# Kernel optimization log

Hardware: AMD Instinct MI355X
Metric: run time of the kernel (lower is better)

## Reference

```python
import jax, jax.numpy as jnp
import numpy as np

IN_FEATURES = 8192
OUT_FEATURES = 8192
WEIGHT_PER_OUT = 32
BATCH = 1024


def setup_inputs() -> dict:
    key = jax.random.key(0)
    k1, k2, k3 = jax.random.split(key, 3)
    x = jax.random.normal(k1, (BATCH, IN_FEATURES), dtype=jnp.float32)
    connections = jax.random.randint(k2, (OUT_FEATURES, WEIGHT_PER_OUT), 0, IN_FEATURES, dtype=jnp.int32)
    bound = 1.0 / np.sqrt(WEIGHT_PER_OUT)
    weights = jax.random.uniform(k3, (OUT_FEATURES, WEIGHT_PER_OUT), dtype=jnp.float32, minval=-bound, maxval=bound)
    return {"x": x, "connections": connections, "weights": weights}


def reference(x, connections, weights):
    # x: [B, In]; connections, weights: [O, K]
    # out[b, o] = sum_k x[b, connections[o, k]] * weights[o, k]
    gathered = jnp.take(x, connections, axis=1)  # [B, O, K]
    return jnp.einsum('bok,ok->bo', gathered, weights)
```

## Files before the change

### kernel.cpp

```cpp
#include <hip/hip_runtime.h>
#include <hip/hip_fp16.h>


typedef _Float16 half2_t __attribute__((ext_vector_type(2)));

constexpr int IN_F    = 8192;
constexpr int OUT_F   = 8192;
constexpr int KPER    = 32;
constexpr int BATCH   = 1024;
constexpr int ROWS    = 4;
constexpr int THREADS = 1024;
constexpr int OHALF   = OUT_F / 2;
constexpr size_t PK_BYTES = (size_t)OUT_F * (KPER / 4) * 16;

__global__ __launch_bounds__(256)
void psl_repack(const int* __restrict__ conn, const float* __restrict__ w,
                uint4* __restrict__ pk) {
    const int t = blockIdx.x * 256 + threadIdx.x;
    const int j = t >> 13;
    const int o = t & (OUT_F - 1);
    const int base = o * KPER + j * 4;
    const int4   ci = *reinterpret_cast<const int4*>(conn + base);
    const float4 wj = *reinterpret_cast<const float4*>(w + base);
    uint4 v;
    v.x = ((unsigned)ci.x << 3) | ((unsigned)ci.y << 19);
    v.z = ((unsigned)ci.z << 3) | ((unsigned)ci.w << 19);
    __half2 w01 = __floats2half2_rn(wj.x, wj.y);
    __half2 w23 = __floats2half2_rn(wj.z, wj.w);
    v.y = *reinterpret_cast<unsigned*>(&w01);
    v.w = *reinterpret_cast<unsigned*>(&w23);
    pk[(size_t)j * OUT_F + o] = v;
}

__device__ __forceinline__ float dot2acc(unsigned hi, unsigned lo,
                                         unsigned sel, unsigned wbits,
                                         float acc) {
    unsigned p = __builtin_amdgcn_perm(hi, lo, sel);
    return __builtin_amdgcn_fdot2(__builtin_bit_cast(half2_t, p),
                                  __builtin_bit_cast(half2_t, wbits),
                                  acc, false);
}

__global__ __launch_bounds__(THREADS, 8)
void psl_main(const float* __restrict__ x, const uint4* __restrict__ pk,
              float* __restrict__ out) {
    __shared__ uint2 lds_x[IN_F];

    const int tid = threadIdx.x;
    const int bt  = blockIdx.x >> 1;
    const int oh  = blockIdx.x & 1;
    const long b0 = (long)bt * ROWS;

    const float* xr0 = x + (b0 + 0) * IN_F;
    const float* xr1 = x + (b0 + 1) * IN_F;
    const float* xr2 = x + (b0 + 2) * IN_F;
    const float* xr3 = x + (b0 + 3) * IN_F;

    for (int c = tid; c < IN_F; c += THREADS) {
        __half2 h01 = __floats2half2_rn(xr0[c], xr1[c]);
        __half2 h23 = __floats2half2_rn(xr2[c], xr3[c]);
        uint2 pkx;
        pkx.x = *reinterpret_cast<unsigned*>(&h01);
        pkx.y = *reinterpret_cast<unsigned*>(&h23);
        lds_x[c] = pkx;
    }
    __syncthreads();

    float* or0 = out + (b0 + 0) * OUT_F;
    float* or1 = out + (b0 + 1) * OUT_F;
    float* or2 = out + (b0 + 2) * OUT_F;
    float* or3 = out + (b0 + 3) * OUT_F;

    const int obase = oh * OHALF;
    const char* ldsb = reinterpret_cast<const char*>(lds_x);

    for (int jj = 0; jj < OHALF / THREADS; ++jj) {
        const int o = obase + jj * THREADS + tid;
        const uint4* pkrow = pk + o;

        float a0 = 0.f, a1 = 0.f, a2 = 0.f, a3 = 0.f;

#pragma unroll 2
        for (int j = 0; j < KPER / 4; ++j) {
            const uint4 v = pkrow[(size_t)j * OUT_F];
            const unsigned off0 = v.x & 0xFFFFu, off1 = v.x >> 16;
            const unsigned off2 = v.z & 0xFFFFu, off3 = v.z >> 16;
            const uint2 g0 = *reinterpret_cast<const uint2*>(ldsb + off0);
            const uint2 g1 = *reinterpret_cast<const uint2*>(ldsb + off1);
            const uint2 g2 = *reinterpret_cast<const uint2*>(ldsb + off2);
            const uint2 g3 = *reinterpret_cast<const uint2*>(ldsb + off3);
            a0 = dot2acc(g1.x, g0.x, 0x05040100u, v.y, a0);
            a1 = dot2acc(g1.x, g0.x, 0x07060302u, v.y, a1);
            a2 = dot2acc(g1.y, g0.y, 0x05040100u, v.y, a2);
            a3 = dot2acc(g1.y, g0.y, 0x07060302u, v.y, a3);
            a0 = dot2acc(g3.x, g2.x, 0x05040100u, v.w, a0);
            a1 = dot2acc(g3.x, g2.x, 0x07060302u, v.w, a1);
            a2 = dot2acc(g3.y, g2.y, 0x05040100u, v.w, a2);
            a3 = dot2acc(g3.y, g2.y, 0x07060302u, v.w, a3);
        }

        or0[o] = a0;
        or1[o] = a1;
        or2[o] = a2;
        or3[o] = a3;
    }
}

__global__ __launch_bounds__(512, 4)
void psl_fallback(const float* __restrict__ x, const int* __restrict__ conn,
                  const float* __restrict__ w, float* __restrict__ out) {
    __shared__ uint2 lds_x[IN_F];
    const int tid = threadIdx.x;
    const int bt  = blockIdx.x >> 1;
    const int oh  = blockIdx.x & 1;
    const long b0 = (long)bt * ROWS;
    const float* xr0 = x + (b0 + 0) * IN_F;
    const float* xr1 = x + (b0 + 1) * IN_F;
    const float* xr2 = x + (b0 + 2) * IN_F;
    const float* xr3 = x + (b0 + 3) * IN_F;
    for (int c = tid; c < IN_F; c += 512) {
        __half2 h01 = __floats2half2_rn(xr0[c], xr1[c]);
        __half2 h23 = __floats2half2_rn(xr2[c], xr3[c]);
        uint2 pkx;
        pkx.x = *reinterpret_cast<unsigned*>(&h01);
        pkx.y = *reinterpret_cast<unsigned*>(&h23);
        lds_x[c] = pkx;
    }
    __syncthreads();
    float* or0 = out + (b0 + 0) * OUT_F;
    float* or1 = out + (b0 + 1) * OUT_F;
    float* or2 = out + (b0 + 2) * OUT_F;
    float* or3 = out + (b0 + 3) * OUT_F;
    const int obase = oh * OHALF;
    for (int j = 0; j < OHALF / 512; ++j) {
        const int o = obase + j * 512 + tid;
        const int4*   c4 = reinterpret_cast<const int4*>(conn + (size_t)o * KPER);
        const float4* w4 = reinterpret_cast<const float4*>(w + (size_t)o * KPER);
        float a0 = 0.f, a1 = 0.f, a2 = 0.f, a3 = 0.f;
#define GACC(IDX, WT)                                              \
        {                                                          \
            uint2 v = lds_x[(IDX)];                                \
            __half2 h01 = *reinterpret_cast<__half2*>(&v.x);       \
            __half2 h23 = *reinterpret_cast<__half2*>(&v.y);       \
            float2 f01 = __half22float2(h01);                      \
            float2 f23 = __half22float2(h23);                      \
            a0 = fmaf(f01.x, (WT), a0);                            \
            a1 = fmaf(f01.y, (WT), a1);                            \
            a2 = fmaf(f23.x, (WT), a2);                            \
            a3 = fmaf(f23.y, (WT), a3);                            \
        }
#pragma unroll
        for (int jj = 0; jj < KPER / 4; ++jj) {
            const int4   ci = c4[jj];
            const float4 wj = w4[jj];
            GACC(ci.x, wj.x);
            GACC(ci.y, wj.y);
            GACC(ci.z, wj.z);
            GACC(ci.w, wj.w);
        }
#undef GACC
        or0[o] = a0;
        or1[o] = a1;
        or2[o] = a2;
        or3[o] = a3;
    }
}

extern "C" void kernel_launch(void* const* d_in, const int* in_sizes, int n_in,
                              void* d_out, int out_size, void* d_ws, size_t ws_size,
                              hipStream_t stream) {
    const float* x    = (const float*)d_in[0];
    const int*   conn = (const int*)d_in[1];
    const float* w    = (const float*)d_in[2];
    float*       out  = (float*)d_out;

    if (ws_size >= PK_BYTES) {
        uint4* pk = (uint4*)d_ws;
        psl_repack<<<dim3(OUT_F * (KPER / 4) / 256), 256, 0, stream>>>(conn, w, pk);
        psl_main<<<dim3((BATCH / ROWS) * 2), THREADS, 0, stream>>>(x, pk, out);
    } else {
        psl_fallback<<<dim3((BATCH / ROWS) * 2), 512, 0, stream>>>(x, conn, w, out);
    }
}
```

Baseline: 104.2 us.

## Process eight batch rows per block with packed fp16 FMA accumulation

Each block now stages eight batch rows of x into LDS as uint4 per input column, so one gathered LDS read serves eight outputs and the packed connection/weight stream is reused across twice as many rows. The fp32 dot2 accumulation with byte permutes is replaced by packed half2 FMAs that accumulate in fp16, split across two accumulator sets and summed in fp32 at the end. This halves the number of blocks and the re-reads of the packed index stream. In exchange it doubles LDS use to 128KB per block, which lowers occupancy, and fp16 accumulation reduces accuracy.

```diff
diff --git a/kernel.cpp b/kernel.cpp
--- a/kernel.cpp
+++ b/kernel.cpp
@@ -1,14 +1,12 @@
 #include <hip/hip_runtime.h>
 #include <hip/hip_fp16.h>
 
-
-typedef _Float16 half2_t __attribute__((ext_vector_type(2)));
 
 constexpr int IN_F    = 8192;
 constexpr int OUT_F   = 8192;
 constexpr int KPER    = 32;
 constexpr int BATCH   = 1024;
-constexpr int ROWS    = 4;
+constexpr int ROWS    = 8;
 constexpr int THREADS = 1024;
 constexpr int OHALF   = OUT_F / 2;
 constexpr size_t PK_BYTES = (size_t)OUT_F * (KPER / 4) * 16;
@@ -23,86 +21,101 @@
     const int4   ci = *reinterpret_cast<const int4*>(conn + base);
     const float4 wj = *reinterpret_cast<const float4*>(w + base);
     uint4 v;
-    v.x = ((unsigned)ci.x << 3) | ((unsigned)ci.y << 19);
-    v.z = ((unsigned)ci.z << 3) | ((unsigned)ci.w << 19);
+    v.x = (unsigned)ci.x | ((unsigned)ci.y << 16);
+    v.y = (unsigned)ci.z | ((unsigned)ci.w << 16);
     __half2 w01 = __floats2half2_rn(wj.x, wj.y);
     __half2 w23 = __floats2half2_rn(wj.z, wj.w);
-    v.y = *reinterpret_cast<unsigned*>(&w01);
+    v.z = *reinterpret_cast<unsigned*>(&w01);
     v.w = *reinterpret_cast<unsigned*>(&w23);
     pk[(size_t)j * OUT_F + o] = v;
 }
 
-__device__ __forceinline__ float dot2acc(unsigned hi, unsigned lo,
-                                         unsigned sel, unsigned wbits,
-                                         float acc) {
-    unsigned p = __builtin_amdgcn_perm(hi, lo, sel);
-    return __builtin_amdgcn_fdot2(__builtin_bit_cast(half2_t, p),
-                                  __builtin_bit_cast(half2_t, wbits),
-                                  acc, false);
+__device__ __forceinline__ __half2 u2h2(unsigned u) {
+    return __builtin_bit_cast(__half2, u);
+}
+__device__ __forceinline__ unsigned packh2(float a, float b) {
+    __half2 h = __floats2half2_rn(a, b);
+    return *reinterpret_cast<unsigned*>(&h);
 }
 
-__global__ __launch_bounds__(THREADS, 8)
+__global__ __launch_bounds__(THREADS, 4)
 void psl_main(const float* __restrict__ x, const uint4* __restrict__ pk,
               float* __restrict__ out) {
-    __shared__ uint2 lds_x[IN_F];
+    __shared__ uint4 lds_x[IN_F];
 
     const int tid = threadIdx.x;
     const int bt  = blockIdx.x >> 1;
     const int oh  = blockIdx.x & 1;
     const long b0 = (long)bt * ROWS;
 
-    const float* xr0 = x + (b0 + 0) * IN_F;
-    const float* xr1 = x + (b0 + 1) * IN_F;
-    const float* xr2 = x + (b0 + 2) * IN_F;
-    const float* xr3 = x + (b0 + 3) * IN_F;
+    const float* xr = x + b0 * IN_F;
 
     for (int c = tid; c < IN_F; c += THREADS) {
-        __half2 h01 = __floats2half2_rn(xr0[c], xr1[c]);
-        __half2 h23 = __floats2half2_rn(xr2[c], xr3[c]);
-        uint2 pkx;
-        pkx.x = *reinterpret_cast<unsigned*>(&h01);
-        pkx.y = *reinterpret_cast<unsigned*>(&h23);
+        uint4 pkx;
+        pkx.x = packh2(xr[0 * IN_F + c], xr[1 * IN_F + c]);
+        pkx.y = packh2(xr[2 * IN_F + c], xr[3 * IN_F + c]);
+        pkx.z = packh2(xr[4 * IN_F + c], xr[5 * IN_F + c]);
+        pkx.w = packh2(xr[6 * IN_F + c], xr[7 * IN_F + c]);
         lds_x[c] = pkx;
     }
     __syncthreads();
 
-    float* or0 = out + (b0 + 0) * OUT_F;
-    float* or1 = out + (b0 + 1) * OUT_F;
-    float* or2 = out + (b0 + 2) * OUT_F;
-    float* or3 = out + (b0 + 3) * OUT_F;
-
+    float* outb = out + b0 * OUT_F;
     const int obase = oh * OHALF;
-    const char* ldsb = reinterpret_cast<const char*>(lds_x);
 
     for (int jj = 0; jj < OHALF / THREADS; ++jj) {
         const int o = obase + jj * THREADS + tid;
         const uint4* pkrow = pk + o;
 
-        float a0 = 0.f, a1 = 0.f, a2 = 0.f, a3 = 0.f;
+        __half2 z = __float2half2_rn(0.f);
+        __half2 a01 = z, a23 = z, a45 = z, a67 = z;
+        __half2 b01 = z, b23 = z, b45 = z, b67 = z;
 
-#pragma unroll 2
+#pragma unroll
         for (int j = 0; j < KPER / 4; ++j) {
             const uint4 v = pkrow[(size_t)j * OUT_F];
-            const unsigned off0 = v.x & 0xFFFFu, off1 = v.x >> 16;
-            const unsigned off2 = v.z & 0xFFFFu, off3 = v.z >> 16;
-            const uint2 g0 = *reinterpret_cast<const uint2*>(ldsb + off0);
-            const uint2 g1 = *reinterpret_cast<const uint2*>(ldsb + off1);
-            const uint2 g2 = *reinterpret_cast<const uint2*>(ldsb + off2);
-            const uint2 g3 = *reinterpret_cast<const uint2*>(ldsb + off3);
-            a0 = dot2acc(g1.x, g0.x, 0x05040100u, v.y, a0);
-            a1 = dot2acc(g1.x, g0.x, 0x07060302u, v.y, a1);
-            a2 = dot2acc(g1.y, g0.y, 0x05040100u, v.y, a2);
-            a3 = dot2acc(g1.y, g0.y, 0x07060302u, v.y, a3);
-            a0 = dot2acc(g3.x, g2.x, 0x05040100u, v.w, a0);
-            a1 = dot2acc(g3.x, g2.x, 0x07060302u, v.w, a1);
-            a2 = dot2acc(g3.y, g2.y, 0x05040100u, v.w, a2);
-            a3 = dot2acc(g3.y, g2.y, 0x07060302u, v.w, a3);
+            const unsigned i0 = v.x & 0xFFFFu, i1 = v.x >> 16;
+            const unsigned i2 = v.y & 0xFFFFu, i3 = v.y >> 16;
+            const uint4 g0 = lds_x[i0];
+            const uint4 g1 = lds_x[i1];
+            const uint4 g2 = lds_x[i2];
+            const uint4 g3 = lds_x[i3];
+            const __half2 w01 = u2h2(v.z), w23 = u2h2(v.w);
+            const __half2 wd0 = __half2half2(__low2half(w01));
+            const __half2 wd1 = __half2half2(__high2half(w01));
+            const __half2 wd2 = __half2half2(__low2half(w23));
+            const __half2 wd3 = __half2half2(__high2half(w23));
+
+            a01 = __hfma2(u2h2(g0.x), wd0, a01);
+            a23 = __hfma2(u2h2(g0.y), wd0, a23);
+            a45 = __hfma2(u2h2(g0.z), wd0, a45);
+            a67 = __hfma2(u2h2(g0.w), wd0, a67);
+            b01 = __hfma2(u2h2(g1.x), wd1, b01);
+            b23 = __hfma2(u2h2(g1.y), wd1, b23);
+            b45 = __hfma2(u2h2(g1.z), wd1, b45);
+            b67 = __hfma2(u2h2(g1.w), wd1, b67);
+            a01 = __hfma2(u2h2(g2.x), wd2, a01);
+            a23 = __hfma2(u2h2(g2.y), wd2, a23);
+            a45 = __hfma2(u2h2(g2.z), wd2, a45);
+            a67 = __hfma2(u2h2(g2.w), wd2, a67);
+            b01 = __hfma2(u2h2(g3.x), wd3, b01);
+            b23 = __hfma2(u2h2(g3.y), wd3, b23);
+            b45 = __hfma2(u2h2(g3.z), wd3, b45);
+            b67 = __hfma2(u2h2(g3.w), wd3, b67);
         }
 
-        or0[o] = a0;
-        or1[o] = a1;
-        or2[o] = a2;
-        or3[o] = a3;
+        const float2 r01 = __half22float2(a01), s01 = __half22float2(b01);
+        const float2 r23 = __half22float2(a23), s23 = __half22float2(b23);
+        const float2 r45 = __half22float2(a45), s45 = __half22float2(b45);
+        const float2 r67 = __half22float2(a67), s67 = __half22float2(b67);
+        outb[0 * OUT_F + o] = r01.x + s01.x;
+        outb[1 * OUT_F + o] = r01.y + s01.y;
+        outb[2 * OUT_F + o] = r23.x + s23.x;
+        outb[3 * OUT_F + o] = r23.y + s23.y;
+        outb[4 * OUT_F + o] = r45.x + s45.x;
+        outb[5 * OUT_F + o] = r45.y + s45.y;
+        outb[6 * OUT_F + o] = r67.x + s67.x;
+        outb[7 * OUT_F + o] = r67.y + s67.y;
     }
 }
 
@@ -113,17 +126,15 @@
     const int tid = threadIdx.x;
     const int bt  = blockIdx.x >> 1;
     const int oh  = blockIdx.x & 1;
-    const long b0 = (long)bt * ROWS;
+    const long b0 = (long)bt * 4;
     const float* xr0 = x + (b0 + 0) * IN_F;
     const float* xr1 = x + (b0 + 1) * IN_F;
     const float* xr2 = x + (b0 + 2) * IN_F;
     const float* xr3 = x + (b0 + 3) * IN_F;
     for (int c = tid; c < IN_F; c += 512) {
-        __half2 h01 = __floats2half2_rn(xr0[c], xr1[c]);
-        __half2 h23 = __floats2half2_rn(xr2[c], xr3[c]);
         uint2 pkx;
-        pkx.x = *reinterpret_cast<unsigned*>(&h01);
-        pkx.y = *reinterpret_cast<unsigned*>(&h23);
+        pkx.x = packh2(xr0[c], xr1[c]);
+        pkx.y = packh2(xr2[c], xr3[c]);
         lds_x[c] = pkx;
     }
     __syncthreads();
@@ -179,6 +190,6 @@
         psl_repack<<<dim3(OUT_F * (KPER / 4) / 256), 256, 0, stream>>>(conn, w, pk);
         psl_main<<<dim3((BATCH / ROWS) * 2), THREADS, 0, stream>>>(x, pk, out);
     } else {
-        psl_fallback<<<dim3((BATCH / ROWS) * 2), 512, 0, stream>>>(x, conn, w, out);
+        psl_fallback<<<dim3((BATCH / 4) * 2), 512, 0, stream>>>(x, conn, w, out);
     }
 }
```

Result: faster. 102.2 us (-2.0%).
